# Kernel tuning notes

Hardware: AMD Instinct MI355X
Metric: run time of the kernel (lower is better)

Reference implementation:

```python
import jax, jax.numpy as jnp
import numpy as np

DIM = 2048
NUM_HEADS = 16
HEAD_DIM = DIM // NUM_HEADS  # 128
LC = HEAD_DIM // 2           # 64 complex pairs per head
B, S = 2, 2048
EPS = 1e-6


def setup_inputs() -> dict:
    key = jax.random.key(0)
    ks = jax.random.split(key, 12)
    x = jax.random.normal(ks[0], (B, S, DIM), dtype=jnp.float32)
    # freqs: unit-modulus complex rotations stored as (cos, sin), shape [S,1,LC,2]
    theta = jax.random.uniform(ks[1], (S, 1, LC), dtype=jnp.float32) * (2.0 * np.pi)
    freqs = jnp.stack([jnp.cos(theta), jnp.sin(theta)], axis=-1)
    scale = 0.02
    wq = jax.random.normal(ks[2], (DIM, DIM), dtype=jnp.float32) * scale
    bq = jnp.zeros((DIM,), dtype=jnp.float32)
    wk = jax.random.normal(ks[3], (DIM, DIM), dtype=jnp.float32) * scale
    bk = jnp.zeros((DIM,), dtype=jnp.float32)
    wv = jax.random.normal(ks[4], (DIM, DIM), dtype=jnp.float32) * scale
    bv = jnp.zeros((DIM,), dtype=jnp.float32)
    wo = jax.random.normal(ks[5], (DIM, DIM), dtype=jnp.float32) * scale
    bo = jnp.zeros((DIM,), dtype=jnp.float32)
    gq = jnp.ones((DIM,), dtype=jnp.float32)   # RMSNorm weight for q
    gk = jnp.ones((DIM,), dtype=jnp.float32)   # RMSNorm weight for k
    return {"x": x, "freqs": freqs, "wq": wq, "bq": bq, "wk": wk, "bk": bk,
            "wv": wv, "bv": bv, "wo": wo, "bo": bo, "gq": gq, "gk": gk}


def _rms_norm(x, g):
    xf = x.astype(jnp.float32)
    y = xf * jax.lax.rsqrt(jnp.mean(xf * xf, axis=-1, keepdims=True) + EPS)
    return y.astype(x.dtype) * g


def _rope_apply(x, freqs):
    # x: [B,S,D] -> complex pairs [B,S,H,LC,2]; freqs: [S,1,LC,2] (cos,sin)
    b, s, _ = x.shape
    xp = x.astype(jnp.float32).reshape(b, s, NUM_HEADS, LC, 2)
    xr, xi = xp[..., 0], xp[..., 1]
    cr = freqs[None, :, :, :, 0]  # [1,S,1,LC]
    ci = freqs[None, :, :, :, 1]
    out_r = xr * cr - xi * ci
    out_i = xr * ci + xi * cr
    out = jnp.stack([out_r, out_i], axis=-1).reshape(b, s, DIM)
    return out.astype(x.dtype)


def _attention(q, k, v):
    # q,k,v: [B,S,D] -> multihead SDPA -> [B,S,D]
    b, s, _ = q.shape
    qh = q.reshape(b, s, NUM_HEADS, HEAD_DIM).transpose(0, 2, 1, 3)
    kh = k.reshape(b, s, NUM_HEADS, HEAD_DIM).transpose(0, 2, 1, 3)
    vh = v.reshape(b, s, NUM_HEADS, HEAD_DIM).transpose(0, 2, 1, 3)
    scale = 1.0 / np.sqrt(HEAD_DIM).astype(np.float32)
    scores = jnp.einsum('bhqd,bhkd->bhqk', qh, kh) * scale
    probs = jax.nn.softmax(scores, axis=-1)
    out = jnp.einsum('bhqk,bhkd->bhqd', probs, vh)
    return out.transpose(0, 2, 1, 3).reshape(b, s, DIM)


def reference(x, freqs, wq, bq, wk, bk, wv, bv, wo, bo, gq, gk):
    q = _rms_norm(x @ wq.T + bq, gq)
    k = _rms_norm(x @ wk.T + bk, gk)
    v = x @ wv.T + bv
    q = _rope_apply(q, freqs)
    k = _rope_apply(k, freqs)
    attn = _attention(q, k, v)
    return attn @ wo.T + bo
```

## Files before the change

### kernel.cpp

```cpp
#include <hip/hip_runtime.h>
#include <cstdint>

typedef __bf16 bf16;
typedef __bf16 bf16x8 __attribute__((ext_vector_type(8)));
typedef __bf16 bf16x4 __attribute__((ext_vector_type(4)));
typedef float f32x4 __attribute__((ext_vector_type(4)));

#define DIMN 2048
#define SEQ  2048
#define NH   16
#define HD   128

__device__ __forceinline__ void gld_lds16(const bf16* g, bf16* l) {
    __builtin_amdgcn_global_load_lds(
        (const __attribute__((address_space(1))) void*)g,
        (__attribute__((address_space(3))) void*)l,
        16, 0, 0);
}

__global__ __launch_bounds__(256) void cast_f32_bf16(const float* __restrict__ src,
                                                     bf16* __restrict__ dst, int n4) {
    int i = blockIdx.x * 256 + threadIdx.x;
    if (i < n4) {
        float4 v = ((const float4*)src)[i];
        bf16x4 o;
        o[0] = (bf16)v.x; o[1] = (bf16)v.y; o[2] = (bf16)v.z; o[3] = (bf16)v.w;
        ((bf16x4*)dst)[i] = o;
    }
}

__global__ __launch_bounds__(256) void cast_w4(
    const float* __restrict__ s0, const float* __restrict__ s1,
    const float* __restrict__ s2, const float* __restrict__ s3,
    bf16* __restrict__ d0, bf16* __restrict__ d1,
    bf16* __restrict__ d2, bf16* __restrict__ d3, int n4) {
    const float* src = s0; bf16* dst = d0;
    if (blockIdx.y == 1) { src = s1; dst = d1; }
    if (blockIdx.y == 2) { src = s2; dst = d2; }
    if (blockIdx.y == 3) { src = s3; dst = d3; }
    int i = blockIdx.x * 256 + threadIdx.x;
    if (i < n4) {
        float4 v = ((const float4*)src)[i];
        bf16x4 o;
        o[0] = (bf16)v.x; o[1] = (bf16)v.y; o[2] = (bf16)v.z; o[3] = (bf16)v.w;
        ((bf16x4*)dst)[i] = o;
    }
}

template<int OUT_F32>
__global__ __launch_bounds__(256) void gemm_bt(
    const bf16* __restrict__ A,
    const bf16* __restrict__ Bw0, const bf16* __restrict__ Bw1, const bf16* __restrict__ Bw2,
    const float* __restrict__ bias0, const float* __restrict__ bias1, const float* __restrict__ bias2,
    void* __restrict__ C0, void* __restrict__ C1, void* __restrict__ C2)
{
    const int K = DIMN, N = DIMN;
    const bf16* Bw = Bw0; const float* bias = bias0; void* Cout = C0;
    if (blockIdx.z == 1) { Bw = Bw1; bias = bias1; Cout = C1; }
    if (blockIdx.z == 2) { Bw = Bw2; bias = bias2; Cout = C2; }

    __shared__ __attribute__((aligned(16))) bf16 As[128 * 64];
    __shared__ __attribute__((aligned(16))) bf16 Bs[128 * 64];

    const int t    = threadIdx.x;
    const int lane = t & 63, wave = t >> 6;
    const int l15  = lane & 15, quad = lane >> 4;
    const int wm   = (wave >> 1) * 64, wn = (wave & 1) * 64;
    const long bm  = (long)blockIdx.y * 128;
    const long bn  = (long)blockIdx.x * 128;

    const bf16* agp[4]; const bf16* bgp[4]; bf16* asd[4]; bf16* bsd[4];
#pragma unroll
    for (int it = 0; it < 4; it++) {
        int fs  = it * 256 + t;
        int row = fs >> 3;
        int gs  = (fs & 7) ^ (row & 7);
        agp[it] = A  + (bm + row) * (long)K + gs * 8;
        bgp[it] = Bw + (bn + row) * (long)K + gs * 8;
        asd[it] = As + fs * 8;
        bsd[it] = Bs + fs * 8;
    }
    const int swl = l15 & 7;

    f32x4 acc[4][4] = {};

    for (int k0 = 0; k0 < K; k0 += 64) {
#pragma unroll
        for (int it = 0; it < 4; it++) {
            gld_lds16(agp[it] + k0, asd[it]);
            gld_lds16(bgp[it] + k0, bsd[it]);
        }
        __syncthreads();

#pragma unroll
        for (int ks2 = 0; ks2 < 2; ks2++) {
            const int sw = ((ks2 * 4 + quad) ^ swl) * 8;
            bf16x8 af[4], bfr[4];
#pragma unroll
            for (int i = 0; i < 4; i++)
                af[i] = *(const bf16x8*)(As + (wm + i * 16 + l15) * 64 + sw);
#pragma unroll
            for (int j = 0; j < 4; j++)
                bfr[j] = *(const bf16x8*)(Bs + (wn + j * 16 + l15) * 64 + sw);
#pragma unroll
            for (int i = 0; i < 4; i++)
#pragma unroll
                for (int j = 0; j < 4; j++)
                    acc[i][j] = __builtin_amdgcn_mfma_f32_16x16x32_bf16(af[i], bfr[j], acc[i][j], 0, 0, 0);
        }
        __syncthreads();
    }

#pragma unroll
    for (int j = 0; j < 4; j++) {
        const long col = bn + wn + j * 16 + l15;
        const float bv = bias[col];
#pragma unroll
        for (int i = 0; i < 4; i++) {
            const long row0 = bm + wm + i * 16 + quad * 4;
#pragma unroll
            for (int r = 0; r < 4; r++) {
                float v = acc[i][j][r] + bv;
                if (OUT_F32) ((float*)Cout)[(row0 + r) * N + col] = v;
                else         ((bf16*)Cout)[(row0 + r) * N + col] = (bf16)v;
            }
        }
    }
}

__global__ __launch_bounds__(256) void rmsnorm_rope(
    bf16* __restrict__ q, bf16* __restrict__ k,
    const float* __restrict__ gq, const float* __restrict__ gk,
    const float* __restrict__ freqs)
{
    const int row = blockIdx.x;
    bf16* ptr = blockIdx.y ? k : q;
    const float* g = blockIdx.y ? gk : gq;
    const float osc = blockIdx.y ? 1.0f : 0.08838834764831845f;
    const int s = row & (SEQ - 1);
    const int t = threadIdx.x;
    const int lane = t & 63, wave = t >> 6;

    bf16* base = ptr + (long)row * DIMN + t * 8;
    bf16x8 raw = *(const bf16x8*)base;
    float v[8]; float ss = 0.f;
#pragma unroll
    for (int j = 0; j < 8; j++) { v[j] = (float)raw[j]; ss += v[j] * v[j]; }
#pragma unroll
    for (int off = 32; off; off >>= 1) ss += __shfl_xor(ss, off, 64);
    __shared__ float red[4];
    if (lane == 0) red[wave] = ss;
    __syncthreads();
    float tot = red[0] + red[1] + red[2] + red[3];
    float rn = rsqrtf(tot * (1.0f / DIMN) + 1e-6f);

    const int e0 = t * 8;
    bf16x8 o;
#pragma unroll
    for (int pp = 0; pp < 4; pp++) {
        int e = e0 + pp * 2;
        float xr = v[pp * 2]     * rn * g[e];
        float xi = v[pp * 2 + 1] * rn * g[e + 1];
        int lc = (e >> 1) & 63;
        float cr = freqs[s * 128 + lc * 2];
        float ci = freqs[s * 128 + lc * 2 + 1];
        o[pp * 2]     = (bf16)((xr * cr - xi * ci) * osc);
        o[pp * 2 + 1] = (bf16)((xr * ci + xi * cr) * osc);
    }
    *(bf16x8*)base = o;
}

__global__ __launch_bounds__(256) void transpose_v(const bf16* __restrict__ vin,
                                                   bf16* __restrict__ vt)
{
    __shared__ float tile[64][65];
    const int b = blockIdx.z, st = blockIdx.x, ct = blockIdx.y;
    const int tx = threadIdx.x & 63, ty = threadIdx.x >> 6;
#pragma unroll
    for (int ii = 0; ii < 16; ii++) {
        int r = ii * 4 + ty;
        tile[r][tx] = (float)vin[((long)(b * SEQ + st * 64 + r)) * DIMN + ct * 64 + tx];
    }
    __syncthreads();
#pragma unroll
    for (int ii = 0; ii < 16; ii++) {
        int c = ii * 4 + ty;
        vt[((long)(b * DIMN + ct * 64 + c)) * SEQ + st * 64 + tx] = (bf16)tile[tx][c];
    }
}

__global__ __launch_bounds__(256, 2) void attention(
    const bf16* __restrict__ Q, const bf16* __restrict__ Kb,
    const bf16* __restrict__ Vt, bf16* __restrict__ O)
{
    __shared__ __attribute__((aligned(16))) bf16 Ksh[64 * 128];
    __shared__ __attribute__((aligned(16))) bf16 Vsh[128 * 64];
    __shared__ __attribute__((aligned(16))) bf16 Psh[4][32 * 72];
    __shared__ float Lsh[4][32];

    const int t = threadIdx.x;
    const int lane = t & 63, wave = t >> 6;
    const int l15 = lane & 15, quad = lane >> 4;
    const int bh = blockIdx.y, b = bh >> 4, h = bh & 15;
    const int qt = blockIdx.x;
    const long qrow0 = (long)b * SEQ + qt * 128 + wave * 32;
    const bf16* qbase = Q  + qrow0 * DIMN + h * HD;
    const bf16* kbase = Kb + (long)b * SEQ * DIMN + h * HD;
    const bf16* vbase = Vt + (long)bh * HD * SEQ;

    bf16x8 qf[2][4];
#pragma unroll
    for (int im = 0; im < 2; im++)
#pragma unroll
        for (int kd = 0; kd < 4; kd++)
            qf[im][kd] = *(const bf16x8*)(qbase + (long)(im * 16 + l15) * DIMN + kd * 32 + quad * 8);

    const bf16* kgp[4]; const bf16* vgp[4]; bf16* ksd[4]; bf16* vsd[4];
#pragma unroll
    for (int it = 0; it < 4; it++) {
        int fs = it * 256 + t;
        int kr = fs >> 4, kp = fs & 15, kks = kp ^ (kr & 15);
        kgp[it] = kbase + (long)kr * DIMN + kks * 8;
        ksd[it] = Ksh + fs * 8;
        int dr = fs >> 3, vp = fs & 7, vks = vp ^ (dr & 7);
        vgp[it] = vbase + (long)dr * SEQ + vks * 8;
        vsd[it] = Vsh + fs * 8;
    }

    f32x4 o_acc[2][8] = {};
    float Lt[2] = {0.f, 0.f};

    for (int kt = 0; kt < 32; kt++) {
#pragma unroll
        for (int it = 0; it < 4; it++) {
            gld_lds16(kgp[it] + (long)(kt * 64) * DIMN, ksd[it]);
            gld_lds16(vgp[it] + kt * 64, vsd[it]);
        }
        __syncthreads();

        f32x4 st[4][2] = {};
#pragma unroll
        for (int jk = 0; jk < 4; jk++)
#pragma unroll
            for (int kd = 0; kd < 4; kd++) {
                bf16x8 kf = *(const bf16x8*)(Ksh + (jk * 16 + l15) * 128 + (((kd * 4 + quad) ^ l15) & 15) * 8);
                st[jk][0] = __builtin_amdgcn_mfma_f32_16x16x32_bf16(kf, qf[0][kd], st[jk][0], 0, 0, 0);
                st[jk][1] = __builtin_amdgcn_mfma_f32_16x16x32_bf16(kf, qf[1][kd], st[jk][1], 0, 0, 0);
            }

#pragma unroll
        for (int im = 0; im < 2; im++) {
            float part = 0.f;
#pragma unroll
            for (int jk = 0; jk < 4; jk++) {
                bf16x4 pk;
#pragma unroll
                for (int r = 0; r < 4; r++) {
                    float e = __expf(st[jk][im][r]);
                    part += e;
                    pk[r] = (bf16)e;
                }
                *(bf16x4*)(Psh[wave] + (im * 16 + l15) * 72 + jk * 16 + quad * 4) = pk;
            }
            part += __shfl_xor(part, 16, 64);
            part += __shfl_xor(part, 32, 64);
            Lt[im] += part;
        }

#pragma unroll
        for (int kd2 = 0; kd2 < 2; kd2++) {
            bf16x8 pa[2];
            pa[0] = *(const bf16x8*)(Psh[wave] + (l15)      * 72 + kd2 * 32 + quad * 8);
            pa[1] = *(const bf16x8*)(Psh[wave] + (16 + l15) * 72 + kd2 * 32 + quad * 8);
#pragma unroll
            for (int dj = 0; dj < 8; dj++) {
                bf16x8 vfr = *(const bf16x8*)(Vsh + (dj * 16 + l15) * 64 + (((kd2 * 4 + quad) ^ l15) & 7) * 8);
                o_acc[0][dj] = __builtin_amdgcn_mfma_f32_16x16x32_bf16(pa[0], vfr, o_acc[0][dj], 0, 0, 0);
                o_acc[1][dj] = __builtin_amdgcn_mfma_f32_16x16x32_bf16(pa[1], vfr, o_acc[1][dj], 0, 0, 0);
            }
        }
        __syncthreads();
    }

    if (quad == 0) { Lsh[wave][l15] = Lt[0]; Lsh[wave][16 + l15] = Lt[1]; }
    __syncthreads();

#pragma unroll
    for (int i = 0; i < 2; i++)
#pragma unroll
        for (int r = 0; r < 4; r++) {
            float inv = 1.0f / Lsh[wave][i * 16 + quad * 4 + r];
            long orow = qrow0 + i * 16 + quad * 4 + r;
#pragma unroll
            for (int dj = 0; dj < 8; dj++)
                O[orow * DIMN + h * HD + dj * 16 + l15] = (bf16)(o_acc[i][dj][r] * inv);
        }
}

extern "C" void kernel_launch(void* const* d_in, const int* in_sizes, int n_in,
                              void* d_out, int out_size, void* d_ws, size_t ws_size,
                              hipStream_t stream) {
    const float* x     = (const float*)d_in[0];
    const float* freqs = (const float*)d_in[1];
    const float* wq    = (const float*)d_in[2];
    const float* bq    = (const float*)d_in[3];
    const float* wk    = (const float*)d_in[4];
    const float* bk    = (const float*)d_in[5];
    const float* wv    = (const float*)d_in[6];
    const float* bv    = (const float*)d_in[7];
    const float* wo    = (const float*)d_in[8];
    const float* bo    = (const float*)d_in[9];
    const float* gq    = (const float*)d_in[10];
    const float* gk    = (const float*)d_in[11];
    float* out = (float*)d_out;

    const size_t MAT  = (size_t)4096 * 2048 * 2;
    const size_t WMAT = (size_t)2048 * 2048 * 2;
    char* p = (char*)d_ws;
    bf16* xb  = (bf16*)p; p += MAT;
    bf16* wqb = (bf16*)p; p += WMAT;
    bf16* wkb = (bf16*)p; p += WMAT;
    bf16* wvb = (bf16*)p; p += WMAT;
    bf16* wob = (bf16*)p; p += WMAT;
    bf16* qb  = (bf16*)p; p += MAT;
    bf16* kb  = (bf16*)p; p += MAT;
    bf16* vb  = (bf16*)p; p += MAT;
    bf16* vt  = (bf16*)p; p += MAT;
    bf16* attn = qb;

    cast_f32_bf16<<<8192, 256, 0, stream>>>(x, xb, 2097152);
    cast_w4<<<dim3(4096, 4), 256, 0, stream>>>(wq, wk, wv, wo, wqb, wkb, wvb, wob, 1048576);

    gemm_bt<0><<<dim3(16, 32, 3), 256, 0, stream>>>(xb, wqb, wkb, wvb,
                                                    bq, bk, bv, qb, kb, vb);
    rmsnorm_rope<<<dim3(4096, 2), 256, 0, stream>>>(qb, kb, gq, gk, freqs);
    transpose_v<<<dim3(32, 32, 2), 256, 0, stream>>>(vb, vt);
    attention<<<dim3(16, 32), 256, 0, stream>>>(qb, kb, vt, attn);
    gemm_bt<1><<<dim3(16, 32, 1), 256, 0, stream>>>(attn, wob, wob, wob,
                                                    bo, bo, bo, out, out, out);
}
```

Before: 411.1 us.

## Use two-wave attention blocks with 64 query rows per wave; merge prep kernels

The attention kernel drops from four waves of 32 query rows to two waves of 64 rows each. Every K and V fragment read from LDS now feeds four MFMA row tiles instead of two, which cuts LDS traffic per flop, and the row-sum shuffles move out of the loop to the end. The two cast kernels are merged into one launch, as are RMSNorm/RoPE and the V transpose. In exchange, the 128-thread attention blocks keep far more accumulator registers per wave and have fewer waves to hide the latency of the K/V loads into LDS.

```diff
diff --git a/kernel.cpp b/kernel.cpp
--- a/kernel.cpp
+++ b/kernel.cpp
@@ -18,33 +18,28 @@
         16, 0, 0);
 }
 
-__global__ __launch_bounds__(256) void cast_f32_bf16(const float* __restrict__ src,
-                                                     bf16* __restrict__ dst, int n4) {
-    int i = blockIdx.x * 256 + threadIdx.x;
-    if (i < n4) {
-        float4 v = ((const float4*)src)[i];
-        bf16x4 o;
-        o[0] = (bf16)v.x; o[1] = (bf16)v.y; o[2] = (bf16)v.z; o[3] = (bf16)v.w;
-        ((bf16x4*)dst)[i] = o;
-    }
-}
-
-__global__ __launch_bounds__(256) void cast_w4(
-    const float* __restrict__ s0, const float* __restrict__ s1,
-    const float* __restrict__ s2, const float* __restrict__ s3,
-    bf16* __restrict__ d0, bf16* __restrict__ d1,
-    bf16* __restrict__ d2, bf16* __restrict__ d3, int n4) {
-    const float* src = s0; bf16* dst = d0;
-    if (blockIdx.y == 1) { src = s1; dst = d1; }
-    if (blockIdx.y == 2) { src = s2; dst = d2; }
-    if (blockIdx.y == 3) { src = s3; dst = d3; }
-    int i = blockIdx.x * 256 + threadIdx.x;
-    if (i < n4) {
-        float4 v = ((const float4*)src)[i];
-        bf16x4 o;
-        o[0] = (bf16)v.x; o[1] = (bf16)v.y; o[2] = (bf16)v.z; o[3] = (bf16)v.w;
-        ((bf16x4*)dst)[i] = o;
-    }
+__global__ __launch_bounds__(256) void cast_all(
+    const float* __restrict__ x,
+    const float* __restrict__ wq, const float* __restrict__ wk,
+    const float* __restrict__ wv, const float* __restrict__ wo,
+    bf16* __restrict__ xb,
+    bf16* __restrict__ wqb, bf16* __restrict__ wkb,
+    bf16* __restrict__ wvb, bf16* __restrict__ wob)
+{
+    int id = blockIdx.x;
+    const float* src; bf16* dst; int i;
+    if (id < 8192) { src = x; dst = xb; i = id * 256 + threadIdx.x; }
+    else {
+        id -= 8192;
+        int w = id >> 12; id &= 4095;
+        src = (w == 0) ? wq : (w == 1) ? wk : (w == 2) ? wv : wo;
+        dst = (w == 0) ? wqb : (w == 1) ? wkb : (w == 2) ? wvb : wob;
+        i = id * 256 + threadIdx.x;
+    }
+    float4 v = ((const float4*)src)[i];
+    bf16x4 o;
+    o[0] = (bf16)v.x; o[1] = (bf16)v.y; o[2] = (bf16)v.z; o[3] = (bf16)v.w;
+    ((bf16x4*)dst)[i] = o;
 }
 
 template<int OUT_F32>
@@ -128,172 +123,184 @@
     }
 }
 
-__global__ __launch_bounds__(256) void rmsnorm_rope(
+__global__ __launch_bounds__(256) void norm_prep(
     bf16* __restrict__ q, bf16* __restrict__ k,
     const float* __restrict__ gq, const float* __restrict__ gk,
-    const float* __restrict__ freqs)
+    const float* __restrict__ freqs,
+    const bf16* __restrict__ vin, bf16* __restrict__ vt)
 {
-    const int row = blockIdx.x;
-    bf16* ptr = blockIdx.y ? k : q;
-    const float* g = blockIdx.y ? gk : gq;
-    const float osc = blockIdx.y ? 1.0f : 0.08838834764831845f;
-    const int s = row & (SEQ - 1);
+    const int id = blockIdx.x;
     const int t = threadIdx.x;
-    const int lane = t & 63, wave = t >> 6;
-
-    bf16* base = ptr + (long)row * DIMN + t * 8;
-    bf16x8 raw = *(const bf16x8*)base;
-    float v[8]; float ss = 0.f;
-#pragma unroll
-    for (int j = 0; j < 8; j++) { v[j] = (float)raw[j]; ss += v[j] * v[j]; }
-#pragma unroll
-    for (int off = 32; off; off >>= 1) ss += __shfl_xor(ss, off, 64);
-    __shared__ float red[4];
-    if (lane == 0) red[wave] = ss;
-    __syncthreads();
-    float tot = red[0] + red[1] + red[2] + red[3];
-    float rn = rsqrtf(tot * (1.0f / DIMN) + 1e-6f);
-
-    const int e0 = t * 8;
-    bf16x8 o;
-#pragma unroll
-    for (int pp = 0; pp < 4; pp++) {
-        int e = e0 + pp * 2;
-        float xr = v[pp * 2]     * rn * g[e];
-        float xi = v[pp * 2 + 1] * rn * g[e + 1];
-        int lc = (e >> 1) & 63;
-        float cr = freqs[s * 128 + lc * 2];
-        float ci = freqs[s * 128 + lc * 2 + 1];
-        o[pp * 2]     = (bf16)((xr * cr - xi * ci) * osc);
-        o[pp * 2 + 1] = (bf16)((xr * ci + xi * cr) * osc);
-    }
-    *(bf16x8*)base = o;
-}
-
-__global__ __launch_bounds__(256) void transpose_v(const bf16* __restrict__ vin,
-                                                   bf16* __restrict__ vt)
-{
-    __shared__ float tile[64][65];
-    const int b = blockIdx.z, st = blockIdx.x, ct = blockIdx.y;
-    const int tx = threadIdx.x & 63, ty = threadIdx.x >> 6;
-#pragma unroll
-    for (int ii = 0; ii < 16; ii++) {
-        int r = ii * 4 + ty;
-        tile[r][tx] = (float)vin[((long)(b * SEQ + st * 64 + r)) * DIMN + ct * 64 + tx];
-    }
-    __syncthreads();
-#pragma unroll
-    for (int ii = 0; ii < 16; ii++) {
-        int c = ii * 4 + ty;
-        vt[((long)(b * DIMN + ct * 64 + c)) * SEQ + st * 64 + tx] = (bf16)tile[tx][c];
-    }
-}
-
-__global__ __launch_bounds__(256, 2) void attention(
+    if (id < 8192) {
+        const int qk  = id >> 12;
+        const int row = id & 4095;
+        bf16* ptr = qk ? k : q;
+        const float* g = qk ? gk : gq;
+        const float osc = qk ? 1.0f : 0.08838834764831845f;
+        const int s = row & (SEQ - 1);
+        const int lane = t & 63, wave = t >> 6;
+
+        bf16* base = ptr + (long)row * DIMN + t * 8;
+        bf16x8 raw = *(const bf16x8*)base;
+        float v[8]; float ss = 0.f;
+#pragma unroll
+        for (int j = 0; j < 8; j++) { v[j] = (float)raw[j]; ss += v[j] * v[j]; }
+#pragma unroll
+        for (int off = 32; off; off >>= 1) ss += __shfl_xor(ss, off, 64);
+        __shared__ float red[4];
+        if (lane == 0) red[wave] = ss;
+        __syncthreads();
+        float tot = red[0] + red[1] + red[2] + red[3];
+        float rn = rsqrtf(tot * (1.0f / DIMN) + 1e-6f);
+
+        const int e0 = t * 8;
+        bf16x8 o;
+#pragma unroll
+        for (int pp = 0; pp < 4; pp++) {
+            int e = e0 + pp * 2;
+            float xr = v[pp * 2]     * rn * g[e];
+            float xi = v[pp * 2 + 1] * rn * g[e + 1];
+            int lc = (e >> 1) & 63;
+            float cr = freqs[s * 128 + lc * 2];
+            float ci = freqs[s * 128 + lc * 2 + 1];
+            o[pp * 2]     = (bf16)((xr * cr - xi * ci) * osc);
+            o[pp * 2 + 1] = (bf16)((xr * ci + xi * cr) * osc);
+        }
+        *(bf16x8*)base = o;
+    } else {
+        const int tid = id - 8192;
+        const int b = tid >> 10, rem = tid & 1023;
+        const int st = rem & 31, ct = rem >> 5;
+        __shared__ float tile[64][65];
+        const int tx = t & 63, ty = t >> 6;
+#pragma unroll
+        for (int ii = 0; ii < 16; ii++) {
+            int r = ii * 4 + ty;
+            tile[r][tx] = (float)vin[((long)(b * SEQ + st * 64 + r)) * DIMN + ct * 64 + tx];
+        }
+        __syncthreads();
+#pragma unroll
+        for (int ii = 0; ii < 16; ii++) {
+            int c = ii * 4 + ty;
+            vt[((long)(b * DIMN + ct * 64 + c)) * SEQ + st * 64 + tx] = (bf16)tile[tx][c];
+        }
+    }
+}
+
+__global__ __launch_bounds__(128, 2) void attention(
     const bf16* __restrict__ Q, const bf16* __restrict__ Kb,
     const bf16* __restrict__ Vt, bf16* __restrict__ O)
 {
     __shared__ __attribute__((aligned(16))) bf16 Ksh[64 * 128];
     __shared__ __attribute__((aligned(16))) bf16 Vsh[128 * 64];
-    __shared__ __attribute__((aligned(16))) bf16 Psh[4][32 * 72];
-    __shared__ float Lsh[4][32];
+    __shared__ __attribute__((aligned(16))) bf16 Psh[2][64 * 72];
+    __shared__ float Lsh[2][64];
 
     const int t = threadIdx.x;
-    const int lane = t & 63, wave = t >> 6;
+    const int lane = t & 63, w = t >> 6;
     const int l15 = lane & 15, quad = lane >> 4;
     const int bh = blockIdx.y, b = bh >> 4, h = bh & 15;
     const int qt = blockIdx.x;
-    const long qrow0 = (long)b * SEQ + qt * 128 + wave * 32;
+    const long qrow0 = (long)b * SEQ + qt * 128 + w * 64;
     const bf16* qbase = Q  + qrow0 * DIMN + h * HD;
     const bf16* kbase = Kb + (long)b * SEQ * DIMN + h * HD;
     const bf16* vbase = Vt + (long)bh * HD * SEQ;
 
-    bf16x8 qf[2][4];
-#pragma unroll
-    for (int im = 0; im < 2; im++)
+    bf16x8 qf[4][4];
+#pragma unroll
+    for (int im = 0; im < 4; im++)
 #pragma unroll
         for (int kd = 0; kd < 4; kd++)
             qf[im][kd] = *(const bf16x8*)(qbase + (long)(im * 16 + l15) * DIMN + kd * 32 + quad * 8);
 
-    const bf16* kgp[4]; const bf16* vgp[4]; bf16* ksd[4]; bf16* vsd[4];
-#pragma unroll
-    for (int it = 0; it < 4; it++) {
-        int fs = it * 256 + t;
-        int kr = fs >> 4, kp = fs & 15, kks = kp ^ (kr & 15);
-        kgp[it] = kbase + (long)kr * DIMN + kks * 8;
-        ksd[it] = Ksh + fs * 8;
-        int dr = fs >> 3, vp = fs & 7, vks = vp ^ (dr & 7);
-        vgp[it] = vbase + (long)dr * SEQ + vks * 8;
-        vsd[it] = Vsh + fs * 8;
-    }
-
-    f32x4 o_acc[2][8] = {};
-    float Lt[2] = {0.f, 0.f};
+    const int t4 = t >> 4;
+    const int kseg0 = (t & 15) ^ t4;
+    const long kb0 = (long)t4 * DIMN + kseg0 * 8;
+    const long kb1 = (long)t4 * DIMN + (kseg0 ^ 8) * 8;
+    const long vb0 = (long)(t >> 3) * SEQ + ((t & 7) ^ ((t >> 3) & 7)) * 8;
+
+    f32x4 o_acc[4][8] = {};
+    float Lt[4] = {0.f, 0.f, 0.f, 0.f};
 
     for (int kt = 0; kt < 32; kt++) {
-#pragma unroll
-        for (int it = 0; it < 4; it++) {
-            gld_lds16(kgp[it] + (long)(kt * 64) * DIMN, ksd[it]);
-            gld_lds16(vgp[it] + kt * 64, vsd[it]);
-        }
-        __syncthreads();
-
-        f32x4 st[4][2] = {};
-#pragma unroll
-        for (int jk = 0; jk < 4; jk++)
-#pragma unroll
-            for (int kd = 0; kd < 4; kd++) {
-                bf16x8 kf = *(const bf16x8*)(Ksh + (jk * 16 + l15) * 128 + (((kd * 4 + quad) ^ l15) & 15) * 8);
-                st[jk][0] = __builtin_amdgcn_mfma_f32_16x16x32_bf16(kf, qf[0][kd], st[jk][0], 0, 0, 0);
-                st[jk][1] = __builtin_amdgcn_mfma_f32_16x16x32_bf16(kf, qf[1][kd], st[jk][1], 0, 0, 0);
+        const bf16* kg = kbase + (long)(kt * 64) * DIMN;
+        const bf16* vg = vbase + kt * 64;
+#pragma unroll
+        for (int it = 0; it < 8; it++) {
+            gld_lds16(kg + (long)it * 8 * DIMN + ((it & 1) ? kb1 : kb0), Ksh + t * 8 + it * 1024);
+            gld_lds16(vg + (long)it * 16 * SEQ + vb0, Vsh + t * 8 + it * 1024);
+        }
+        __syncthreads();
+
+#pragma unroll
+        for (int jp = 0; jp < 2; jp++) {
+            f32x4 st[2][4] = {};
+#pragma unroll
+            for (int jj = 0; jj < 2; jj++) {
+                const int jk = jp * 2 + jj;
+#pragma unroll
+                for (int kd = 0; kd < 4; kd++) {
+                    bf16x8 kf = *(const bf16x8*)(Ksh + (jk * 16 + l15) * 128 + (((kd * 4 + quad) ^ l15) & 15) * 8);
+#pragma unroll
+                    for (int im = 0; im < 4; im++)
+                        st[jj][im] = __builtin_amdgcn_mfma_f32_16x16x32_bf16(kf, qf[im][kd], st[jj][im], 0, 0, 0);
+                }
             }
-
-#pragma unroll
-        for (int im = 0; im < 2; im++) {
-            float part = 0.f;
-#pragma unroll
-            for (int jk = 0; jk < 4; jk++) {
-                bf16x4 pk;
-#pragma unroll
-                for (int r = 0; r < 4; r++) {
-                    float e = __expf(st[jk][im][r]);
-                    part += e;
-                    pk[r] = (bf16)e;
+#pragma unroll
+            for (int jj = 0; jj < 2; jj++) {
+                const int jk = jp * 2 + jj;
+#pragma unroll
+                for (int im = 0; im < 4; im++) {
+                    bf16x4 pk;
+                    float part = 0.f;
+#pragma unroll
+                    for (int r = 0; r < 4; r++) {
+                        float e = __expf(st[jj][im][r]);
+                        part += e;
+                        pk[r] = (bf16)e;
+                    }
+                    *(bf16x4*)(Psh[w] + (im * 16 + l15) * 72 + jk * 16 + quad * 4) = pk;
+                    Lt[im] += part;
                 }
-                *(bf16x4*)(Psh[wave] + (im * 16 + l15) * 72 + jk * 16 + quad * 4) = pk;
             }
-            part += __shfl_xor(part, 16, 64);
-            part += __shfl_xor(part, 32, 64);
-            Lt[im] += part;
         }
 
 #pragma unroll
         for (int kd2 = 0; kd2 < 2; kd2++) {
-            bf16x8 pa[2];
-            pa[0] = *(const bf16x8*)(Psh[wave] + (l15)      * 72 + kd2 * 32 + quad * 8);
-            pa[1] = *(const bf16x8*)(Psh[wave] + (16 + l15) * 72 + kd2 * 32 + quad * 8);
+            bf16x8 pa[4];
+#pragma unroll
+            for (int im = 0; im < 4; im++)
+                pa[im] = *(const bf16x8*)(Psh[w] + (im * 16 + l15) * 72 + kd2 * 32 + quad * 8);
 #pragma unroll
             for (int dj = 0; dj < 8; dj++) {
                 bf16x8 vfr = *(const bf16x8*)(Vsh + (dj * 16 + l15) * 64 + (((kd2 * 4 + quad) ^ l15) & 7) * 8);
-                o_acc[0][dj] = __builtin_amdgcn_mfma_f32_16x16x32_bf16(pa[0], vfr, o_acc[0][dj], 0, 0, 0);
-                o_acc[1][dj] = __builtin_amdgcn_mfma_f32_16x16x32_bf16(pa[1], vfr, o_acc[1][dj], 0, 0, 0);
+#pragma unroll
+                for (int im = 0; im < 4; im++)
+                    o_acc[im][dj] = __builtin_amdgcn_mfma_f32_16x16x32_bf16(pa[im], vfr, o_acc[im][dj], 0, 0, 0);
             }
         }
         __syncthreads();
     }
 
-    if (quad == 0) { Lsh[wave][l15] = Lt[0]; Lsh[wave][16 + l15] = Lt[1]; }
+#pragma unroll
+    for (int im = 0; im < 4; im++) {
+        Lt[im] += __shfl_xor(Lt[im], 16, 64);
+        Lt[im] += __shfl_xor(Lt[im], 32, 64);
+    }
+    if (quad == 0)
+#pragma unroll
+        for (int im = 0; im < 4; im++) Lsh[w][im * 16 + l15] = Lt[im];
     __syncthreads();
 
 #pragma unroll
-    for (int i = 0; i < 2; i++)
+    for (int im = 0; im < 4; im++)
 #pragma unroll
         for (int r = 0; r < 4; r++) {
-            float inv = 1.0f / Lsh[wave][i * 16 + quad * 4 + r];
-            long orow = qrow0 + i * 16 + quad * 4 + r;
+            float inv = 1.0f / Lsh[w][im * 16 + quad * 4 + r];
+            long orow = qrow0 + im * 16 + quad * 4 + r;
 #pragma unroll
             for (int dj = 0; dj < 8; dj++)
-                O[orow * DIMN + h * HD + dj * 16 + l15] = (bf16)(o_acc[i][dj][r] * inv);
+                O[orow * DIMN + h * HD + dj * 16 + l15] = (bf16)(o_acc[im][dj][r] * inv);
         }
 }
 
@@ -328,14 +335,12 @@
     bf16* vt  = (bf16*)p; p += MAT;
     bf16* attn = qb;
 
-    cast_f32_bf16<<<8192, 256, 0, stream>>>(x, xb, 2097152);
-    cast_w4<<<dim3(4096, 4), 256, 0, stream>>>(wq, wk, wv, wo, wqb, wkb, wvb, wob, 1048576);
+    cast_all<<<24576, 256, 0, stream>>>(x, wq, wk, wv, wo, xb, wqb, wkb, wvb, wob);
 
     gemm_bt<0><<<dim3(16, 32, 3), 256, 0, stream>>>(xb, wqb, wkb, wvb,
                                                     bq, bk, bv, qb, kb, vb);
-    rmsnorm_rope<<<dim3(4096, 2), 256, 0, stream>>>(qb, kb, gq, gk, freqs);
-    transpose_v<<<dim3(32, 32, 2), 256, 0, stream>>>(vb, vt);
-    attention<<<dim3(16, 32), 256, 0, stream>>>(qb, kb, vt, attn);
+    norm_prep<<<10240, 256, 0, stream>>>(qb, kb, gq, gk, freqs, vb, vt);
+    attention<<<dim3(16, 32), 128, 0, stream>>>(qb, kb, vt, attn);
     gemm_bt<1><<<dim3(16, 32, 1), 256, 0, stream>>>(attn, wob, wob, wob,
                                                     bo, bo, bo, out, out, out);
 }
```

Result: slower. 501.6 us (+22.0%).
